# Performance work log

Hardware: AMD Instinct MI355X
Metric: run time of the kernel (lower is better)

The kernel has to match this reference:

```python
import jax, jax.numpy as jnp
import numpy as np
import math

B, LQ, LK = 2, 2048, 2048
DIM = 1024
H = 16
DH = DIM // H


def setup_inputs() -> dict:
    key = jax.random.key(0)
    ks = jax.random.split(key, 12)
    s = 1.0 / math.sqrt(DIM)
    return {
        "query": jax.random.normal(ks[0], (B, LQ, DIM), jnp.float32),
        "key": jax.random.normal(ks[1], (B, LK, DIM), jnp.float32),
        "value": jax.random.normal(ks[2], (B, LK, DIM), jnp.float32),
        "mask": jnp.zeros((B, LQ, LK), dtype=bool),
        "Wq": jax.random.normal(ks[3], (DIM, DIM), jnp.float32) * s,
        "bq": jax.random.normal(ks[4], (DIM,), jnp.float32) * s,
        "Wk": jax.random.normal(ks[5], (DIM, DIM), jnp.float32) * s,
        "bk": jax.random.normal(ks[6], (DIM,), jnp.float32) * s,
        "Wv": jax.random.normal(ks[7], (DIM, DIM), jnp.float32) * s,
        "bv": jax.random.normal(ks[8], (DIM,), jnp.float32) * s,
        "Wo": jax.random.normal(ks[9], (DIM, DIM), jnp.float32) * s,
        "bo": jax.random.normal(ks[10], (DIM,), jnp.float32) * s,
    }


def reference(query, key, value, mask, Wq, bq, Wk, bk, Wv, bv, Wo, bo):
    b = query.shape[0]

    def shape(x):  # (b, l, dim) -> (b, h, l, dh)
        return x.reshape(b, -1, H, DH).transpose(0, 2, 1, 3)

    q = shape(query @ Wq.T + bq)
    k = shape(key @ Wk.T + bk)
    v = shape(value @ Wv.T + bv)

    q = q / math.sqrt(DH)
    # (b, h, lq, lk) score matrix, computed in float32 as the original does
    scores = jnp.einsum("bhqd,bhkd->bhqk", q, k).astype(jnp.float32)
    scores = jnp.where(mask[:, None, :, :], jnp.float32(-1e18), scores)
    attn = jax.nn.softmax(scores, axis=-1).astype(q.dtype)
    context = jnp.einsum("bhqk,bhkd->bhqd", attn, v)
    context = context.transpose(0, 2, 1, 3).reshape(b, -1, H * DH)
    return context @ Wo.T + bo
```

## Files before the change

### kernel.cpp

```cpp
#include <hip/hip_runtime.h>
#include <hip/hip_bf16.h>

typedef __attribute__((ext_vector_type(4))) float float4v;
typedef __attribute__((ext_vector_type(8))) __bf16 bf16x8;
typedef __attribute__((ext_vector_type(4))) unsigned short ushort4v;

#define MFMA16(a, b, c) __builtin_amdgcn_mfma_f32_16x16x32_bf16(a, b, c, 0, 0, 0)

__device__ __forceinline__ unsigned short f2bf(float f) {
    return __builtin_bit_cast(unsigned short, (__bf16)f);
}

__device__ __forceinline__ float fast_exp2(float x) {
#if __has_builtin(__builtin_amdgcn_exp2f)
    return __builtin_amdgcn_exp2f(x);
#else
    return exp2f(x);
#endif
}

__device__ __forceinline__ void gl_lds16(const unsigned short* g, unsigned short* l) {
    __builtin_amdgcn_global_load_lds(
        (const __attribute__((address_space(1))) void*)g,
        (__attribute__((address_space(3))) void*)l, 16, 0, 0);
}

struct CvtSeg { const float* s; unsigned short* d; int n; };
struct Cvt7 { CvtSeg seg[7]; };

__global__ __launch_bounds__(256) void cvt_kernel(Cvt7 a) {
    const CvtSeg c = a.seg[blockIdx.y];
    const int stride = gridDim.x * 256 * 4;
    for (int i = (blockIdx.x * 256 + threadIdx.x) * 4; i < c.n; i += stride) {
        float4v v = *(const float4v*)(c.s + i);
        ushort4v u;
        u.x = f2bf(v.x); u.y = f2bf(v.y); u.z = f2bf(v.z); u.w = f2bf(v.w);
        *(ushort4v*)(c.d + i) = u;
    }
}

__device__ __forceinline__ void gemm128_body(const unsigned short* __restrict__ A,
                                             const unsigned short* __restrict__ W,
                                             const float* __restrict__ bias,
                                             unsigned short* __restrict__ Cout,
                                             int N, int K, float scale,
                                             unsigned short* As, unsigned short* Ws) {
    const int t = threadIdx.x;
    const int w = t >> 6, lane = t & 63;
    const int quad = lane >> 4, l16 = lane & 15;
    const int m0 = blockIdx.x * 128, n0 = blockIdx.y * 128;
    const int wm = (w >> 1) * 64, wn = (w & 1) * 64;

    float4v acc[4][4];
    for (int i = 0; i < 4; ++i)
        for (int j = 0; j < 4; ++j) acc[i][j] = float4v{0.f, 0.f, 0.f, 0.f};

    const int srow = lane >> 3;
    const int scol = (lane & 7) * 8;

    for (int k0 = 0; k0 < K; k0 += 64) {
        __syncthreads();
        for (int i = 0; i < 4; ++i) {
            const int c = w * 4 + i;
            gl_lds16(A + (size_t)(m0 + c * 8 + srow) * K + k0 + scol,
                     &As[c * 512 + lane * 8]);
            gl_lds16(W + (size_t)(n0 + c * 8 + srow) * K + k0 + scol,
                     &Ws[c * 512 + lane * 8]);
        }
        __syncthreads();
        for (int ks = 0; ks < 2; ++ks) {
            bf16x8 af[4], wf[4];
            for (int i = 0; i < 4; ++i)
                af[i] = *(const bf16x8*)&As[(wm + i * 16 + l16) * 64 + ks * 32 + quad * 8];
            for (int i = 0; i < 4; ++i)
                wf[i] = *(const bf16x8*)&Ws[(wn + i * 16 + l16) * 64 + ks * 32 + quad * 8];
            for (int mi = 0; mi < 4; ++mi)
                for (int ni = 0; ni < 4; ++ni)
                    acc[mi][ni] = MFMA16(af[mi], wf[ni], acc[mi][ni]);
        }
    }

    for (int mi = 0; mi < 4; ++mi)
        for (int ni = 0; ni < 4; ++ni) {
            const int col = n0 + wn + ni * 16 + l16;
            const float bv = bias[col];
            for (int reg = 0; reg < 4; ++reg) {
                const int row = m0 + wm + mi * 16 + quad * 4 + reg;
                Cout[(size_t)row * N + col] = f2bf((acc[mi][ni][reg] + bv) * scale);
            }
        }
}

__global__ __launch_bounds__(256) void gemm_qkv_kernel(
    const unsigned short* qa, const unsigned short* ka, const unsigned short* va,
    const unsigned short* Wqb, const unsigned short* Wkb, const unsigned short* Wvb,
    const float* bq, const float* bk, const float* bv,
    unsigned short* Qb, unsigned short* Kb, unsigned short* Vb, float qscale) {
    __shared__ unsigned short As[128 * 64];
    __shared__ unsigned short Ws[128 * 64];
    const int z = blockIdx.z;
    const unsigned short* A = z == 0 ? qa : (z == 1 ? ka : va);
    const unsigned short* W = z == 0 ? Wqb : (z == 1 ? Wkb : Wvb);
    const float* bias = z == 0 ? bq : (z == 1 ? bk : bv);
    unsigned short* C = z == 0 ? Qb : (z == 1 ? Kb : Vb);
    gemm128_body(A, W, bias, C, 1024, 1024, z == 0 ? qscale : 1.0f, As, Ws);
}

__global__ __launch_bounds__(256) void gemm_out_kernel(const unsigned short* __restrict__ A,
                                                       const unsigned short* __restrict__ W,
                                                       const float* __restrict__ bias,
                                                       float* __restrict__ Cout) {
    __shared__ unsigned short As[64 * 64];
    __shared__ unsigned short Ws[128 * 64];
    const int N = 1024, K = 1024;
    const int t = threadIdx.x;
    const int w = t >> 6, lane = t & 63;
    const int quad = lane >> 4, l16 = lane & 15;
    const int m0 = blockIdx.x * 64, n0 = blockIdx.y * 128;
    const int wm = (w & 1) * 32, wn = (w >> 1) * 64;

    float4v acc[2][4];
    for (int i = 0; i < 2; ++i)
        for (int j = 0; j < 4; ++j) acc[i][j] = float4v{0.f, 0.f, 0.f, 0.f};

    const int srow = lane >> 3;
    const int scol = (lane & 7) * 8;

    for (int k0 = 0; k0 < K; k0 += 64) {
        __syncthreads();
        for (int i = 0; i < 2; ++i) {
            const int c = w * 2 + i;
            gl_lds16(A + (size_t)(m0 + c * 8 + srow) * K + k0 + scol,
                     &As[c * 512 + lane * 8]);
        }
        for (int i = 0; i < 4; ++i) {
            const int c = w * 4 + i;
            gl_lds16(W + (size_t)(n0 + c * 8 + srow) * K + k0 + scol,
                     &Ws[c * 512 + lane * 8]);
        }
        __syncthreads();
        for (int ks = 0; ks < 2; ++ks) {
            bf16x8 af[2], wf[4];
            for (int i = 0; i < 2; ++i)
                af[i] = *(const bf16x8*)&As[(wm + i * 16 + l16) * 64 + ks * 32 + quad * 8];
            for (int i = 0; i < 4; ++i)
                wf[i] = *(const bf16x8*)&Ws[(wn + i * 16 + l16) * 64 + ks * 32 + quad * 8];
            for (int mi = 0; mi < 2; ++mi)
                for (int ni = 0; ni < 4; ++ni)
                    acc[mi][ni] = MFMA16(af[mi], wf[ni], acc[mi][ni]);
        }
    }

    for (int mi = 0; mi < 2; ++mi)
        for (int ni = 0; ni < 4; ++ni) {
            const int col = n0 + wn + ni * 16 + l16;
            const float bv = bias[col];
            for (int reg = 0; reg < 4; ++reg) {
                const int row = m0 + wm + mi * 16 + quad * 4 + reg;
                Cout[(size_t)row * N + col] = acc[mi][ni][reg] + bv;
            }
        }
}

__global__ __launch_bounds__(256) void attn_kernel(const unsigned short* __restrict__ Q,
                                                   const unsigned short* __restrict__ Kg,
                                                   const unsigned short* __restrict__ Vg,
                                                   const unsigned char* __restrict__ mask,
                                                   float* __restrict__ Op,
                                                   float* __restrict__ Lp) {
    const int bid = blockIdx.x;
    const int bh = bid & 31;
    const int sp = (bid >> 5) & 1;
    const int qt = bid >> 6;
    const int b = bh >> 4, h = bh & 15;
    const int t = threadIdx.x, w = t >> 6, lane = t & 63;
    const int quad = lane >> 4, l16 = lane & 15;

    __shared__ unsigned short Ps[128][72];
    __shared__ unsigned short Ks[64][72];
    __shared__ unsigned short Vt[80][72];

    const int kbase = sp * 1024;
    const unsigned short* Qp = Q + ((size_t)(b * 2048 + qt * 128)) * 1024 + h * 64;
    const unsigned short* Kp = Kg + ((size_t)(b * 2048 + kbase)) * 1024 + h * 64;
    const unsigned short* Vp = Vg + ((size_t)(b * 2048 + kbase)) * 1024 + h * 64;
    const unsigned char* Mp = mask + (size_t)(b * 2048 + qt * 128) * 2048 + kbase;

    for (int idx = t; idx < 16 * 72; idx += 256) {
        const int r = idx / 72, c = idx - r * 72;
        Vt[64 + r][c] = (r == 0) ? (unsigned short)0x3F80 : (unsigned short)0;
    }
    for (int p = 0; p < 4; ++p) {
        const int idx = t + p * 256;
        const int r = idx >> 3, c8 = (idx & 7) * 8;
        *(uint4*)&Ps[r][c8] = *(const uint4*)(Qp + (size_t)r * 1024 + c8);
    }
    __syncthreads();
    bf16x8 qf[2][2];
    for (int c = 0; c < 2; ++c)
        for (int ks = 0; ks < 2; ++ks)
            qf[c][ks] = *(const bf16x8*)&Ps[w * 32 + c * 16 + l16][ks * 32 + quad * 8];

    float4v o[2][5];
    for (int c = 0; c < 2; ++c)
        for (int i = 0; i < 5; ++i) o[c][i] = float4v{0.f, 0.f, 0.f, 0.f};

    const int sr = t >> 3, sc8 = (t & 7) * 8;
    const int vkk = (t & 31) * 2, vd0 = (t >> 5) * 8;
    const int mrow = w * 32 + (lane >> 1);
    const int mc0 = (lane & 1) * 32;

    uint4 kreg0, kreg1, vreg0, vreg1, mreg0, mreg1;
    {
        kreg0 = *(const uint4*)(Kp + (size_t)sr * 1024 + sc8);
        kreg1 = *(const uint4*)(Kp + (size_t)(sr + 32) * 1024 + sc8);
        vreg0 = *(const uint4*)(Vp + (size_t)vkk * 1024 + vd0);
        vreg1 = *(const uint4*)(Vp + (size_t)(vkk + 1) * 1024 + vd0);
        mreg0 = *(const uint4*)(Mp + (size_t)mrow * 2048 + mc0);
        mreg1 = *(const uint4*)(Mp + (size_t)mrow * 2048 + mc0 + 16);
    }

    for (int kc = 0; kc < 1024; kc += 64) {
        __syncthreads();
        *(uint4*)&Ks[sr][sc8] = kreg0;
        *(uint4*)&Ks[sr + 32][sc8] = kreg1;
        {
            const unsigned short* pa = (const unsigned short*)&vreg0;
            const unsigned short* pb = (const unsigned short*)&vreg1;
            for (int j = 0; j < 8; ++j)
                *(unsigned int*)&Vt[vd0 + j][vkk] =
                    (unsigned int)pa[j] | ((unsigned int)pb[j] << 16);
        }
        const unsigned int mor = mreg0.x | mreg0.y | mreg0.z | mreg0.w |
                                 mreg1.x | mreg1.y | mreg1.z | mreg1.w;
        const bool anymask = __any(mor != 0);
        __syncthreads();

        const int kn = kc + 64;
        if (kn < 1024) {
            kreg0 = *(const uint4*)(Kp + (size_t)(kn + sr) * 1024 + sc8);
            kreg1 = *(const uint4*)(Kp + (size_t)(kn + sr + 32) * 1024 + sc8);
            vreg0 = *(const uint4*)(Vp + (size_t)(kn + vkk) * 1024 + vd0);
            vreg1 = *(const uint4*)(Vp + (size_t)(kn + vkk + 1) * 1024 + vd0);
            mreg0 = *(const uint4*)(Mp + (size_t)mrow * 2048 + kn + mc0);
            mreg1 = *(const uint4*)(Mp + (size_t)mrow * 2048 + kn + mc0 + 16);
        }

        float4v s0[4], s1[4];
        for (int nt = 0; nt < 4; ++nt) {
            const float4v z4 = float4v{0.f, 0.f, 0.f, 0.f};
            bf16x8 kf = *(const bf16x8*)&Ks[nt * 16 + l16][quad * 8];
            s0[nt] = MFMA16(qf[0][0], kf, z4);
            s1[nt] = MFMA16(qf[1][0], kf, z4);
            kf = *(const bf16x8*)&Ks[nt * 16 + l16][32 + quad * 8];
            s0[nt] = MFMA16(qf[0][1], kf, s0[nt]);
            s1[nt] = MFMA16(qf[1][1], kf, s1[nt]);
        }

        for (int c = 0; c < 2; ++c) {
            float4v* s = c ? s1 : s0;
            for (int reg = 0; reg < 4; ++reg) {
                float sv[4];
                for (int nt = 0; nt < 4; ++nt) sv[nt] = s[nt][reg];
                if (anymask) {
                    const unsigned char* mr =
                        Mp + (size_t)(w * 32 + c * 16 + quad * 4 + reg) * 2048 + kc;
                    for (int nt = 0; nt < 4; ++nt)
                        if (mr[nt * 16 + l16]) sv[nt] = -1e18f;
                }
                for (int nt = 0; nt < 4; ++nt)
                    Ps[w * 32 + c * 16 + quad * 4 + reg][nt * 16 + l16] =
                        f2bf(fast_exp2(sv[nt]));
            }
        }

        bf16x8 pf0[2], pf1[2];
        for (int ks = 0; ks < 2; ++ks) {
            pf0[ks] = *(const bf16x8*)&Ps[w * 32 + l16][ks * 32 + quad * 8];
            pf1[ks] = *(const bf16x8*)&Ps[w * 32 + 16 + l16][ks * 32 + quad * 8];
        }
        for (int ks = 0; ks < 2; ++ks)
            for (int dt = 0; dt < 5; ++dt) {
                bf16x8 vf = *(const bf16x8*)&Vt[dt * 16 + l16][ks * 32 + quad * 8];
                o[0][dt] = MFMA16(pf0[ks], vf, o[0][dt]);
                o[1][dt] = MFMA16(pf1[ks], vf, o[1][dt]);
            }
    }

    float* Opp = Op + (size_t)sp * 4096 * 1024;
    float* Lpp = Lp + (size_t)sp * 65536;
    for (int c = 0; c < 2; ++c) {
        for (int reg = 0; reg < 4; ++reg) {
            const int ql = w * 32 + c * 16 + quad * 4 + reg;
            const int grow = b * 2048 + qt * 128 + ql;
            if (l16 == 0) Lpp[(size_t)grow * 16 + h] = o[c][4][reg];
        }
        for (int dt = 0; dt < 4; ++dt) {
            const int dcol = dt * 16 + l16;
            for (int reg = 0; reg < 4; ++reg) {
                const int ql = w * 32 + c * 16 + quad * 4 + reg;
                const int grow = b * 2048 + qt * 128 + ql;
                Opp[(size_t)grow * 1024 + h * 64 + dcol] = o[c][dt][reg];
            }
        }
    }
}

__global__ __launch_bounds__(256) void combine_kernel(const float* __restrict__ Op,
                                                      const float* __restrict__ Lp,
                                                      unsigned short* __restrict__ Cb) {
    const size_t e = ((size_t)blockIdx.x * 256 + threadIdx.x) * 4;
    const int row = (int)(e >> 10);
    const int h = ((int)e & 1023) >> 6;
    float4v a = *(const float4v*)(Op + e);
    float4v bq = *(const float4v*)(Op + (size_t)4096 * 1024 + e);
    const float inv = 1.0f / (Lp[(size_t)row * 16 + h] + Lp[65536 + (size_t)row * 16 + h]);
    ushort4v u;
    u.x = f2bf((a.x + bq.x) * inv);
    u.y = f2bf((a.y + bq.y) * inv);
    u.z = f2bf((a.z + bq.z) * inv);
    u.w = f2bf((a.w + bq.w) * inv);
    *(ushort4v*)(Cb + e) = u;
}

extern "C" void kernel_launch(void* const* d_in, const int* in_sizes, int n_in,
                              void* d_out, int out_size, void* d_ws, size_t ws_size,
                              hipStream_t stream) {
    (void)in_sizes; (void)n_in; (void)out_size; (void)ws_size;
    const float* query = (const float*)d_in[0];
    const float* key   = (const float*)d_in[1];
    const float* value = (const float*)d_in[2];
    const unsigned char* mask = (const unsigned char*)d_in[3];
    const float* Wq = (const float*)d_in[4];
    const float* bq = (const float*)d_in[5];
    const float* Wk = (const float*)d_in[6];
    const float* bk = (const float*)d_in[7];
    const float* Wv = (const float*)d_in[8];
    const float* bv = (const float*)d_in[9];
    const float* Wo = (const float*)d_in[10];
    const float* bo = (const float*)d_in[11];

    const size_t MD = (size_t)4096 * 1024;
    const size_t WD = (size_t)1024 * 1024;

    unsigned short* Qb  = (unsigned short*)d_ws;
    unsigned short* Kb  = Qb + MD;
    unsigned short* Vb  = Kb + MD;
    unsigned short* qb  = Vb + MD;
    unsigned short* kb  = qb + MD;
    unsigned short* vb  = kb + MD;
    unsigned short* Wqb = vb + MD;
    unsigned short* Wkb = Wqb + WD;
    unsigned short* Wvb = Wkb + WD;
    float* Op = (float*)qb;
    unsigned short* Wob = qb + 4 * MD;
    unsigned short* Cb  = Wob + WD;
    float* Lp = (float*)(Cb + MD);

    Cvt7 cv;
    cv.seg[0] = {query, qb, (int)MD};
    cv.seg[1] = {key,   kb, (int)MD};
    cv.seg[2] = {value, vb, (int)MD};
    cv.seg[3] = {Wq, Wqb, (int)WD};
    cv.seg[4] = {Wk, Wkb, (int)WD};
    cv.seg[5] = {Wv, Wvb, (int)WD};
    cv.seg[6] = {Wo, Wob, (int)WD};
    cvt_kernel<<<dim3(1024, 7), 256, 0, stream>>>(cv);

    const float qscale = 0.125f * 1.44269504088896f;
    gemm_qkv_kernel<<<dim3(32, 8, 3), 256, 0, stream>>>(
        qb, kb, vb, Wqb, Wkb, Wvb, bq, bk, bv, Qb, Kb, Vb, qscale);

    attn_kernel<<<dim3(1024), 256, 0, stream>>>(Qb, Kb, Vb, mask, Op, Lp);

    combine_kernel<<<dim3(4096), 256, 0, stream>>>(Op, Lp, Cb);

    gemm_out_kernel<<<dim3(64, 8), 256, 0, stream>>>(Cb, Wob, bo, (float*)d_out);
}
```

Before: 276.2 us.

## Halve attention query tile and compute row sums with VALU shuffles

The attention kernel now processes 64 query rows per block instead of 128, with each wave owning one 16-row MFMA tile, and the grid doubles to 2048 blocks. The ones-column trick that folded the softmax denominator into the PV MFMA (the fifth Vt tile) is replaced by summing exponentials in registers and reducing across lanes with shuffles at the end. This cuts registers and LDS per block, which should raise occupancy, and drops one fifth of the PV MFMAs. In exchange, K/V tiles are staged twice as often per query row, so global and LDS traffic for K and V grows.

```diff
diff --git a/kernel.cpp b/kernel.cpp
--- a/kernel.cpp
+++ b/kernel.cpp
@@ -176,48 +176,42 @@
     const int t = threadIdx.x, w = t >> 6, lane = t & 63;
     const int quad = lane >> 4, l16 = lane & 15;
 
-    __shared__ unsigned short Ps[128][72];
+    __shared__ unsigned short Ps[64][72];
     __shared__ unsigned short Ks[64][72];
-    __shared__ unsigned short Vt[80][72];
+    __shared__ unsigned short Vt[64][72];
 
     const int kbase = sp * 1024;
-    const unsigned short* Qp = Q + ((size_t)(b * 2048 + qt * 128)) * 1024 + h * 64;
+    const unsigned short* Qp = Q + ((size_t)(b * 2048 + qt * 64)) * 1024 + h * 64;
     const unsigned short* Kp = Kg + ((size_t)(b * 2048 + kbase)) * 1024 + h * 64;
     const unsigned short* Vp = Vg + ((size_t)(b * 2048 + kbase)) * 1024 + h * 64;
-    const unsigned char* Mp = mask + (size_t)(b * 2048 + qt * 128) * 2048 + kbase;
-
-    for (int idx = t; idx < 16 * 72; idx += 256) {
-        const int r = idx / 72, c = idx - r * 72;
-        Vt[64 + r][c] = (r == 0) ? (unsigned short)0x3F80 : (unsigned short)0;
-    }
-    for (int p = 0; p < 4; ++p) {
-        const int idx = t + p * 256;
-        const int r = idx >> 3, c8 = (idx & 7) * 8;
+    const unsigned char* Mp = mask + (size_t)(b * 2048 + qt * 64) * 2048 + kbase;
+
+    {
+        const int r = t >> 3, c8 = (t & 7) * 8;
         *(uint4*)&Ps[r][c8] = *(const uint4*)(Qp + (size_t)r * 1024 + c8);
+        *(uint4*)&Ps[r + 32][c8] = *(const uint4*)(Qp + (size_t)(r + 32) * 1024 + c8);
     }
     __syncthreads();
-    bf16x8 qf[2][2];
-    for (int c = 0; c < 2; ++c)
-        for (int ks = 0; ks < 2; ++ks)
-            qf[c][ks] = *(const bf16x8*)&Ps[w * 32 + c * 16 + l16][ks * 32 + quad * 8];
-
-    float4v o[2][5];
-    for (int c = 0; c < 2; ++c)
-        for (int i = 0; i < 5; ++i) o[c][i] = float4v{0.f, 0.f, 0.f, 0.f};
+    bf16x8 qf[2];
+    qf[0] = *(const bf16x8*)&Ps[w * 16 + l16][quad * 8];
+    qf[1] = *(const bf16x8*)&Ps[w * 16 + l16][32 + quad * 8];
+
+    float4v o[4];
+    for (int i = 0; i < 4; ++i) o[i] = float4v{0.f, 0.f, 0.f, 0.f};
+    float4v l_acc = float4v{0.f, 0.f, 0.f, 0.f};
 
     const int sr = t >> 3, sc8 = (t & 7) * 8;
     const int vkk = (t & 31) * 2, vd0 = (t >> 5) * 8;
-    const int mrow = w * 32 + (lane >> 1);
-    const int mc0 = (lane & 1) * 32;
-
-    uint4 kreg0, kreg1, vreg0, vreg1, mreg0, mreg1;
+    const int mrow = w * 16 + (lane >> 2);
+    const int mc0 = (lane & 3) * 16;
+
+    uint4 kreg0, kreg1, vreg0, vreg1, mreg;
     {
         kreg0 = *(const uint4*)(Kp + (size_t)sr * 1024 + sc8);
         kreg1 = *(const uint4*)(Kp + (size_t)(sr + 32) * 1024 + sc8);
         vreg0 = *(const uint4*)(Vp + (size_t)vkk * 1024 + vd0);
         vreg1 = *(const uint4*)(Vp + (size_t)(vkk + 1) * 1024 + vd0);
-        mreg0 = *(const uint4*)(Mp + (size_t)mrow * 2048 + mc0);
-        mreg1 = *(const uint4*)(Mp + (size_t)mrow * 2048 + mc0 + 16);
+        mreg  = *(const uint4*)(Mp + (size_t)mrow * 2048 + mc0);
     }
 
     for (int kc = 0; kc < 1024; kc += 64) {
@@ -231,9 +225,7 @@
                 *(unsigned int*)&Vt[vd0 + j][vkk] =
                     (unsigned int)pa[j] | ((unsigned int)pb[j] << 16);
         }
-        const unsigned int mor = mreg0.x | mreg0.y | mreg0.z | mreg0.w |
-                                 mreg1.x | mreg1.y | mreg1.z | mreg1.w;
-        const bool anymask = __any(mor != 0);
+        const bool anymask = __any((mreg.x | mreg.y | mreg.z | mreg.w) != 0);
         __syncthreads();
 
         const int kn = kc + 64;
@@ -242,66 +234,66 @@
             kreg1 = *(const uint4*)(Kp + (size_t)(kn + sr + 32) * 1024 + sc8);
             vreg0 = *(const uint4*)(Vp + (size_t)(kn + vkk) * 1024 + vd0);
             vreg1 = *(const uint4*)(Vp + (size_t)(kn + vkk + 1) * 1024 + vd0);
-            mreg0 = *(const uint4*)(Mp + (size_t)mrow * 2048 + kn + mc0);
-            mreg1 = *(const uint4*)(Mp + (size_t)mrow * 2048 + kn + mc0 + 16);
-        }
-
-        float4v s0[4], s1[4];
+            mreg  = *(const uint4*)(Mp + (size_t)mrow * 2048 + kn + mc0);
+        }
+
+        float4v s[4];
         for (int nt = 0; nt < 4; ++nt) {
             const float4v z4 = float4v{0.f, 0.f, 0.f, 0.f};
             bf16x8 kf = *(const bf16x8*)&Ks[nt * 16 + l16][quad * 8];
-            s0[nt] = MFMA16(qf[0][0], kf, z4);
-            s1[nt] = MFMA16(qf[1][0], kf, z4);
+            s[nt] = MFMA16(qf[0], kf, z4);
             kf = *(const bf16x8*)&Ks[nt * 16 + l16][32 + quad * 8];
-            s0[nt] = MFMA16(qf[0][1], kf, s0[nt]);
-            s1[nt] = MFMA16(qf[1][1], kf, s1[nt]);
-        }
-
-        for (int c = 0; c < 2; ++c) {
-            float4v* s = c ? s1 : s0;
-            for (int reg = 0; reg < 4; ++reg) {
-                float sv[4];
-                for (int nt = 0; nt < 4; ++nt) sv[nt] = s[nt][reg];
-                if (anymask) {
-                    const unsigned char* mr =
-                        Mp + (size_t)(w * 32 + c * 16 + quad * 4 + reg) * 2048 + kc;
-                    for (int nt = 0; nt < 4; ++nt)
-                        if (mr[nt * 16 + l16]) sv[nt] = -1e18f;
-                }
+            s[nt] = MFMA16(qf[1], kf, s[nt]);
+        }
+
+        for (int reg = 0; reg < 4; ++reg) {
+            float sv[4];
+            for (int nt = 0; nt < 4; ++nt) sv[nt] = s[nt][reg];
+            if (anymask) {
+                const unsigned char* mr =
+                    Mp + (size_t)(w * 16 + quad * 4 + reg) * 2048 + kc;
                 for (int nt = 0; nt < 4; ++nt)
-                    Ps[w * 32 + c * 16 + quad * 4 + reg][nt * 16 + l16] =
-                        f2bf(fast_exp2(sv[nt]));
-            }
-        }
-
-        bf16x8 pf0[2], pf1[2];
+                    if (mr[nt * 16 + l16]) sv[nt] = -1e18f;
+            }
+            float rs = 0.f;
+            for (int nt = 0; nt < 4; ++nt) {
+                const float pe = fast_exp2(sv[nt]);
+                rs += pe;
+                Ps[w * 16 + quad * 4 + reg][nt * 16 + l16] = f2bf(pe);
+            }
+            l_acc[reg] += rs;
+        }
+
         for (int ks = 0; ks < 2; ++ks) {
-            pf0[ks] = *(const bf16x8*)&Ps[w * 32 + l16][ks * 32 + quad * 8];
-            pf1[ks] = *(const bf16x8*)&Ps[w * 32 + 16 + l16][ks * 32 + quad * 8];
-        }
-        for (int ks = 0; ks < 2; ++ks)
-            for (int dt = 0; dt < 5; ++dt) {
+            bf16x8 pf = *(const bf16x8*)&Ps[w * 16 + l16][ks * 32 + quad * 8];
+            for (int dt = 0; dt < 4; ++dt) {
                 bf16x8 vf = *(const bf16x8*)&Vt[dt * 16 + l16][ks * 32 + quad * 8];
-                o[0][dt] = MFMA16(pf0[ks], vf, o[0][dt]);
-                o[1][dt] = MFMA16(pf1[ks], vf, o[1][dt]);
-            }
+                o[dt] = MFMA16(pf, vf, o[dt]);
+            }
+        }
+    }
+
+    float lr[4];
+    for (int reg = 0; reg < 4; ++reg) {
+        float l = l_acc[reg];
+        l += __shfl_xor(l, 1);
+        l += __shfl_xor(l, 2);
+        l += __shfl_xor(l, 4);
+        l += __shfl_xor(l, 8);
+        lr[reg] = l;
     }
 
     float* Opp = Op + (size_t)sp * 4096 * 1024;
     float* Lpp = Lp + (size_t)sp * 65536;
-    for (int c = 0; c < 2; ++c) {
+    for (int reg = 0; reg < 4; ++reg) {
+        const int grow = b * 2048 + qt * 64 + w * 16 + quad * 4 + reg;
+        if (l16 == 0) Lpp[(size_t)grow * 16 + h] = lr[reg];
+    }
+    for (int dt = 0; dt < 4; ++dt) {
+        const int dcol = dt * 16 + l16;
         for (int reg = 0; reg < 4; ++reg) {
-            const int ql = w * 32 + c * 16 + quad * 4 + reg;
-            const int grow = b * 2048 + qt * 128 + ql;
-            if (l16 == 0) Lpp[(size_t)grow * 16 + h] = o[c][4][reg];
-        }
-        for (int dt = 0; dt < 4; ++dt) {
-            const int dcol = dt * 16 + l16;
-            for (int reg = 0; reg < 4; ++reg) {
-                const int ql = w * 32 + c * 16 + quad * 4 + reg;
-                const int grow = b * 2048 + qt * 128 + ql;
-                Opp[(size_t)grow * 1024 + h * 64 + dcol] = o[c][dt][reg];
-            }
+            const int grow = b * 2048 + qt * 64 + w * 16 + quad * 4 + reg;
+            Opp[(size_t)grow * 1024 + h * 64 + dcol] = o[dt][reg];
         }
     }
 }
@@ -371,7 +363,7 @@
     gemm_qkv_kernel<<<dim3(32, 8, 3), 256, 0, stream>>>(
         qb, kb, vb, Wqb, Wkb, Wvb, bq, bk, bv, Qb, Kb, Vb, qscale);
 
-    attn_kernel<<<dim3(1024), 256, 0, stream>>>(Qb, Kb, Vb, mask, Op, Lp);
+    attn_kernel<<<dim3(2048), 256, 0, stream>>>(Qb, Kb, Vb, mask, Op, Lp);
 
     combine_kernel<<<dim3(4096), 256, 0, stream>>>(Op, Lp, Cb);
 
```

New measurement: 282.9 us. 2.4% more time.
